# Kernel optimization log

Measured on AMD Instinct MI355X. Metric: run time of the kernel, lower is better.

## Reference

```python
import jax, jax.numpy as jnp
import numpy as np

N = 10000      # num_nodes
E = 80000      # num_edges
IN = 256       # input_dim
T = 768        # text_embedding_dim
H1, H2 = 1024, 1024
HEADS = 4
ND = 100       # num_domains
NS = 10000     # num_skills
SD = 128       # skill_dim
B = 1024       # skill batch
K = 20         # skills per set
LN_EPS = 1e-5
COS_EPS = 1e-8
NEG_SLOPE = 0.2


def setup_inputs() -> dict:
    key = jax.random.key(0)
    ks = jax.random.split(key, 64)
    r = lambda i, shape, s=0.02: jax.random.normal(ks[i], shape, jnp.float32) * s
    inp = {}
    inp['x'] = jax.random.normal(ks[0], (N, IN), jnp.float32)
    inp['edge_index'] = jax.random.randint(ks[1], (2, E), 0, N)
    inp['domain_ids'] = jax.random.randint(ks[2], (N,), 0, ND)
    inp['skill_ids_1'] = jax.random.randint(ks[3], (B, K), 0, NS)
    inp['skill_ids_2'] = jax.random.randint(ks[4], (B, K), 0, NS)
    for j, name in enumerate(['bio', 'expertise', 'needs', 'goals']):
        inp[name + '_embeddings'] = jax.random.normal(ks[5 + j], (N, T), jnp.float32)
        inp[name + '_w'] = r(9 + 2 * j, (T, T))
        inp[name + '_b'] = jnp.zeros((T,), jnp.float32)
    dims = [IN + 4 * T, H1, H2]
    for i in range(2):
        din, dout = dims[i], dims[i + 1]
        base = 20 + 8 * i
        inp[f'gcn_w{i}'] = r(base, (din, dout))
        inp[f'gcn_b{i}'] = jnp.zeros((dout,), jnp.float32)
        inp[f'gat_w{i}'] = r(base + 1, (dout, dout))
        inp[f'gat_as{i}'] = r(base + 2, (HEADS, dout // HEADS), 0.1)
        inp[f'gat_ad{i}'] = r(base + 3, (HEADS, dout // HEADS), 0.1)
        inp[f'gat_b{i}'] = jnp.zeros((dout,), jnp.float32)
        inp[f'ln_g{i}'] = jnp.ones((dout,), jnp.float32)
        inp[f'ln_b{i}'] = jnp.zeros((dout,), jnp.float32)
    inp['dom_emb'] = r(40, (ND, H2), 1.0)
    inp['dom_w'] = r(41, (H2, H2))
    inp['dom_b'] = jnp.zeros((H2,), jnp.float32)
    inp['skill_emb'] = r(42, (NS, SD), 1.0)
    inp['c_w1'] = r(43, (2 * SD, H2))
    inp['c_b1'] = jnp.zeros((H2,), jnp.float32)
    inp['c_w2'] = r(44, (H2, 1))
    inp['c_b2'] = jnp.zeros((1,), jnp.float32)
    return inp


def _layernorm(x, g, b):
    m = x.mean(-1, keepdims=True)
    v = ((x - m) ** 2).mean(-1, keepdims=True)
    return (x - m) * jax.lax.rsqrt(v + LN_EPS) * g + b


def _gcn(x, src, dst, W, b, n):
    # PyG GCNConv: self loops already in (src,dst); symmetric normalization
    xw = x @ W
    deg = jnp.zeros((n,), x.dtype).at[dst].add(1.0)
    dinv = jax.lax.rsqrt(jnp.maximum(deg, 1.0))  # deg >= 1 due to self loops
    norm = dinv[src] * dinv[dst]                 # [Etot]
    out = jnp.zeros_like(xw).at[dst].add(norm[:, None] * xw[src])
    return out + b


def _gat(x, src, dst, W, a_s, a_d, b, n, heads):
    c = W.shape[1] // heads
    h = (x @ W).reshape(n, heads, c)             # [N,H,C]
    es = jnp.einsum('nhc,hc->nh', h, a_s)
    ed = jnp.einsum('nhc,hc->nh', h, a_d)
    e = jax.nn.leaky_relu(es[src] + ed[dst], NEG_SLOPE)   # [Etot,H]
    m = jnp.full((n, heads), -jnp.inf, x.dtype).at[dst].max(e)
    ee = jnp.exp(e - m[dst])
    s = jnp.zeros((n, heads), x.dtype).at[dst].add(ee)
    alpha = ee / s[dst]                          # segment softmax over dst
    out = jnp.zeros((n, heads, c), x.dtype).at[dst].add(alpha[..., None] * h[src])
    return out.reshape(n, heads * c) + b


def _cos(a, b):
    na = jnp.maximum(jnp.linalg.norm(a, axis=-1), COS_EPS)
    nb = jnp.maximum(jnp.linalg.norm(b, axis=-1), COS_EPS)
    return (a * b).sum(-1) / (na * nb)


def _forward(x, edge_index, domain_ids, skill_ids_1, skill_ids_2,
             bio_embeddings, bio_w, bio_b,
             expertise_embeddings, expertise_w, expertise_b,
             needs_embeddings, needs_w, needs_b,
             goals_embeddings, goals_w, goals_b,
             gcn_w0, gcn_b0, gat_w0, gat_as0, gat_ad0, gat_b0, ln_g0, ln_b0,
             gcn_w1, gcn_b1, gat_w1, gat_as1, gat_ad1, gat_b1, ln_g1, ln_b1,
             dom_emb, dom_w, dom_b, skill_emb, c_w1, c_b1, c_w2, c_b2):
    n = x.shape[0]
    bio_f = bio_embeddings @ bio_w + bio_b
    exp_f = expertise_embeddings @ expertise_w + expertise_b
    needs_f = needs_embeddings @ needs_w + needs_b
    goals_f = goals_embeddings @ goals_w + goals_b
    combined = jnp.concatenate([x, bio_f, exp_f, needs_f, goals_f], axis=1)

    src, dst = edge_index[0], edge_index[1]
    loops = jnp.arange(n)
    srcl = jnp.concatenate([src, loops])   # self loops (GCN & GAT both add them)
    dstl = jnp.concatenate([dst, loops])

    h = combined
    layers = [(gcn_w0, gcn_b0, gat_w0, gat_as0, gat_ad0, gat_b0, ln_g0, ln_b0),
              (gcn_w1, gcn_b1, gat_w1, gat_as1, gat_ad1, gat_b1, ln_g1, ln_b1)]
    for (gw, gb, aw, a_s, a_d, ab, lg, lb) in layers:
        x_gcn = _gcn(h, srcl, dstl, gw, gb, n)
        x_att = _gat(x_gcn, srcl, dstl, aw, a_s, a_d, ab, n, HEADS)
        h = jax.nn.relu(_layernorm(x_att + x_gcn, lg, lb))

    domain_embeddings = h @ dom_w + dom_b + dom_emb[domain_ids]

    s1 = skill_emb[skill_ids_1].mean(axis=1)   # [B,SD]
    s2 = skill_emb[skill_ids_2].mean(axis=1)
    comb = jnp.concatenate([s1, s2], axis=1)
    compat = jax.nn.sigmoid(jax.nn.relu(comb @ c_w1 + c_b1) @ c_w2 + c_b2)

    bio_sim = _cos(bio_f[src], bio_f[dst])
    en_sim = _cos(exp_f[src], needs_f[dst])
    ne_sim = _cos(needs_f[src], exp_f[dst])
    goals_sim = _cos(goals_f[src], goals_f[dst])
    return domain_embeddings, compat, bio_sim, en_sim, ne_sim, goals_sim


def reference(x, edge_index, domain_ids, skill_ids_1, skill_ids_2,
              bio_embeddings, bio_w, bio_b,
              expertise_embeddings, expertise_w, expertise_b,
              needs_embeddings, needs_w, needs_b,
              goals_embeddings, goals_w, goals_b,
              gcn_w0, gcn_b0, gat_w0, gat_as0, gat_ad0, gat_b0, ln_g0, ln_b0,
              gcn_w1, gcn_b1, gat_w1, gat_as1, gat_ad1, gat_b1, ln_g1, ln_b1,
              dom_emb, dom_w, dom_b, skill_emb, c_w1, c_b1, c_w2, c_b2):
    return _forward(x, edge_index, domain_ids, skill_ids_1, skill_ids_2,
                    bio_embeddings, bio_w, bio_b,
                    expertise_embeddings, expertise_w, expertise_b,
                    needs_embeddings, needs_w, needs_b,
                    goals_embeddings, goals_w, goals_b,
                    gcn_w0, gcn_b0, gat_w0, gat_as0, gat_ad0, gat_b0, ln_g0, ln_b0,
                    gcn_w1, gcn_b1, gat_w1, gat_as1, gat_ad1, gat_b1, ln_g1, ln_b1,
                    dom_emb, dom_w, dom_b, skill_emb, c_w1, c_b1, c_w2, c_b2)
```

## Files before the change

kernel.cpp:

```cpp
#include <hip/hip_runtime.h>
#include <math.h>

typedef unsigned short u16;
typedef unsigned short u16x4 __attribute__((ext_vector_type(4)));
typedef unsigned short u16x8 __attribute__((ext_vector_type(8)));
typedef short s16x8 __attribute__((ext_vector_type(8)));
typedef float f32x4 __attribute__((ext_vector_type(4)));

constexpr int NN   = 10000;
constexpr int MP   = 10112;
constexpr int IN   = 256;
constexpr int TD   = 768;
constexpr int CD   = 3328;
constexpr int HD   = 1024;
constexpr int HCH  = 256;
constexpr int SDIM = 128;
constexpr int KSK  = 20;
constexpr int ACAP = 256;
constexpr float LN_EPS = 1e-5f;
constexpr float COS_EPS = 1e-8f;
constexpr float NEG_SLOPE = 0.2f;

__device__ __forceinline__ float warp_sum(float v){
#pragma unroll
  for (int o=1;o<64;o<<=1) v += __shfl_xor(v,o);
  return v;
}
__device__ __forceinline__ float warp_max(float v){
#pragma unroll
  for (int o=1;o<64;o<<=1) v = fmaxf(v, __shfl_xor(v,o));
  return v;
}
__device__ __forceinline__ u16 f2b(float f){
  unsigned u = __float_as_uint(f);
  return (u16)((u + 0x7fffu + ((u>>16)&1u)) >> 16);
}
__device__ __forceinline__ float b2f(u16 b){ return __uint_as_float(((unsigned)b)<<16); }

#define GLDS(g, l) __builtin_amdgcn_global_load_lds( \
    (const __attribute__((address_space(1))) void*)(g), \
    (__attribute__((address_space(3))) void*)(l), 16, 0, 0)

__global__ __launch_bounds__(256) void k_gemm_bf16(
    const u16* __restrict__ A, long Az,
    const u16* __restrict__ B0c, const u16* __restrict__ B1c,
    const u16* __restrict__ B2c, const u16* __restrict__ B3c,
    const float* __restrict__ bias0, const float* __restrict__ bias1,
    const float* __restrict__ bias2, const float* __restrict__ bias3,
    float* __restrict__ Cf, int ldcf,
    u16* __restrict__ Cb, int ldcb, long Cbz,
    const float* __restrict__ demb, const int* __restrict__ dids,
    int M, int K, int relu)
{
  __shared__ __align__(16) u16 smem[16384];
  const int z = blockIdx.z;
  const u16* Bt = (z==0)? B0c : (z==1)? B1c : (z==2)? B2c : B3c;
  const float* bias = (z==0)? bias0 : (z==1)? bias1 : (z==2)? bias2 : bias3;
  const u16* Ab = A + (size_t)z * (size_t)Az;

  const int tid = threadIdx.x;
  const int wave = tid >> 6, lane = tid & 63;
  const int wr = wave >> 1, wc = wave & 1;

  const int nwg  = gridDim.x * gridDim.y;
  const int orig = blockIdx.y * gridDim.x + blockIdx.x;
  const int q = nwg >> 3, r = nwg & 7;
  const int xcd = orig & 7, loc = orig >> 3;
  const int wg = (xcd < r ? xcd*(q+1) : r*(q+1) + (xcd-r)*q) + loc;
  const int bx = wg % gridDim.x, byy = wg / gridDim.x;
  const size_t bm = (size_t)byy * 128;
  const size_t bn = (size_t)bx * 128;

  f32x4 acc[4][4];
#pragma unroll
  for (int m=0;m<4;m++)
#pragma unroll
    for (int n=0;n<4;n++) acc[m][n] = f32x4{0.f,0.f,0.f,0.f};

  const int srow = tid >> 2;
  const int scol = (tid & 3) * 8;
  const u16* ga0 = Ab + (bm + srow) * (size_t)K + scol;
  const u16* ga1 = ga0 + (size_t)64 * K;
  const u16* gb0 = Bt + (bn + srow) * (size_t)K + scol;
  const u16* gb1 = gb0 + (size_t)64 * K;

  auto stage = [&](int buf, int k0){
    GLDS(ga0 + k0, smem + buf*4096 + wave*512);
    GLDS(ga1 + k0, smem + buf*4096 + 2048 + wave*512);
    GLDS(gb0 + k0, smem + 8192 + buf*4096 + wave*512);
    GLDS(gb1 + k0, smem + 8192 + buf*4096 + 2048 + wave*512);
  };

  const int ar = wr*64 + (lane & 15);
  const int br = wc*64 + (lane & 15);
  const int kg = (lane >> 4) * 8;

  const int nt = K >> 5;
  stage(0, 0);
  __syncthreads();
  int cur = 0;
  for (int t = 0; t < nt; ++t){
    if (t+1 < nt) stage(cur^1, (t+1)*32);
    s16x8 a[4], b[4];
#pragma unroll
    for (int m=0;m<4;m++) a[m] = *(const s16x8*)(smem + cur*4096 + (ar + m*16)*32 + kg);
#pragma unroll
    for (int n=0;n<4;n++) b[n] = *(const s16x8*)(smem + 8192 + cur*4096 + (br + n*16)*32 + kg);
#pragma unroll
    for (int m=0;m<4;m++)
#pragma unroll
      for (int n=0;n<4;n++)
        acc[m][n] = __builtin_amdgcn_mfma_f32_16x16x32_bf16(a[m], b[n], acc[m][n], 0, 0, 0);
    __syncthreads();
    cur ^= 1;
  }

  const int cl0 = wc*64 + (lane & 15);
  if (Cb){
#pragma unroll
    for (int m=0;m<4;m++)
#pragma unroll
      for (int j=0;j<4;j++){
        int rl = wr*64 + ((lane >> 4) * 4) + m*16 + j;
#pragma unroll
        for (int n=0;n<4;n++){
          int cl = cl0 + n*16;
          float v = acc[m][n][j];
          if (bias) v += bias[bn + cl];
          if (relu) v = fmaxf(v, 0.f);
          smem[rl*128 + cl] = f2b(v);
        }
      }
    __syncthreads();
#pragma unroll
    for (int it=0; it<8; ++it){
      int rl = it*16 + (tid >> 4);
      int cl = (tid & 15) * 8;
      u16x8 vv = *(const u16x8*)(smem + rl*128 + cl);
      *(u16x8*)(Cb + (size_t)z*Cbz + (bm + rl)*(size_t)ldcb + bn + cl) = vv;
    }
  } else if (Cf){
    float* ctf = (float*)smem;
#pragma unroll
    for (int p=0;p<2;p++){
      if (wr == p){
#pragma unroll
        for (int m=0;m<4;m++)
#pragma unroll
          for (int j=0;j<4;j++){
            int rl = ((lane >> 4) * 4) + m*16 + j;
            int rg = (int)bm + p*64 + rl;
            const float* dbase = (demb && rg < M) ? demb + (size_t)dids[rg]*HD : nullptr;
#pragma unroll
            for (int n=0;n<4;n++){
              int cl = cl0 + n*16;
              float v = acc[m][n][j];
              if (bias) v += bias[bn + cl];
              if (dbase) v += dbase[bn + cl];
              if (relu) v = fmaxf(v, 0.f);
              ctf[rl*128 + cl] = v;
            }
          }
      }
      __syncthreads();
#pragma unroll
      for (int it=0; it<8; ++it){
        int rl = it*8 + (tid >> 5);
        int cl = (tid & 31) * 4;
        int rg = (int)bm + p*64 + rl;
        if (rg < M){
          float4 vv = *(const float4*)(ctf + rl*128 + cl);
          *(float4*)(Cf + (size_t)rg*ldcf + bn + cl) = vv;
        }
      }
      __syncthreads();
    }
  }
}

__global__ void k_f2b8x4(const float* __restrict__ s0, const float* __restrict__ s1,
                         const float* __restrict__ s2, const float* __restrict__ s3,
                         u16* __restrict__ out, long per, long ostride){
  int z = blockIdx.y;
  const float* s = (z==0)? s0 : (z==1)? s1 : (z==2)? s2 : s3;
  long i = ((long)blockIdx.x*256 + threadIdx.x)*8;
  if (i >= per) return;
  float4 v0 = *(const float4*)(s+i);
  float4 v1 = *(const float4*)(s+i+4);
  u16x8 o;
  o[0]=f2b(v0.x); o[1]=f2b(v0.y); o[2]=f2b(v0.z); o[3]=f2b(v0.w);
  o[4]=f2b(v1.x); o[5]=f2b(v1.y); o[6]=f2b(v1.z); o[7]=f2b(v1.w);
  *(u16x8*)(out + z*ostride + i) = o;
}

__global__ void k_copyx_b(const float* __restrict__ x, u16* __restrict__ comb){
  long i = ((long)blockIdx.x*256 + threadIdx.x)*8;
  int n = (int)(i >> 8), c = (int)(i & 255);
  float4 v0 = *(const float4*)(x+i);
  float4 v1 = *(const float4*)(x+i+4);
  u16x8 o;
  o[0]=f2b(v0.x); o[1]=f2b(v0.y); o[2]=f2b(v0.z); o[3]=f2b(v0.w);
  o[4]=f2b(v1.x); o[5]=f2b(v1.y); o[6]=f2b(v1.z); o[7]=f2b(v1.w);
  *(u16x8*)(comb + (size_t)n*CD + c) = o;
}

__global__ __launch_bounds__(256) void k_transb4(
    const float* __restrict__ B0c, const float* __restrict__ B1c,
    const float* __restrict__ B2c, const float* __restrict__ B3c,
    u16* __restrict__ T0, u16* __restrict__ T1,
    u16* __restrict__ T2, u16* __restrict__ T3, int K, int N){
  __shared__ u16 tile[32][40];
  int z = blockIdx.z;
  const float* B = (z==0)? B0c : (z==1)? B1c : (z==2)? B2c : B3c;
  u16* Bt = (z==0)? T0 : (z==1)? T1 : (z==2)? T2 : T3;
  int n0 = blockIdx.x*32, k0 = blockIdx.y*32;
  int tx = threadIdx.x & 31, ty = threadIdx.x >> 5;
#pragma unroll
  for (int i=0;i<4;i++)
    tile[ty+8*i][tx] = f2b(B[(size_t)(k0+ty+8*i)*N + n0+tx]);
  __syncthreads();
#pragma unroll
  for (int i=0;i<4;i++)
    Bt[(size_t)(n0+ty+8*i)*K + k0+tx] = tile[tx][ty+8*i];
}

__global__ void k_hist(const int* __restrict__ dst, int* __restrict__ indeg, int E){
  int e = blockIdx.x*256 + threadIdx.x;
  if (e < E) atomicAdd(&indeg[dst[e]], 1);
}

__global__ __launch_bounds__(1024) void k_scan(const int* __restrict__ indeg,
    int* __restrict__ row_start, int* __restrict__ cursor,
    float* __restrict__ dinv, int Nn)
{
  __shared__ int wsum[16];
  __shared__ int carry_s;
  int t = threadIdx.x, wave = t >> 6, lane = t & 63;
  if (t==0) carry_s = 0;
  __syncthreads();
  for (int base=0; base<Nn; base+=1024) {
    int i = base + t;
    int v = (i<Nn)? indeg[i] : 0;
    int s = v;
#pragma unroll
    for (int o=1;o<64;o<<=1){ int tmp = __shfl_up(s, o); if (lane>=o) s += tmp; }
    if (lane==63) wsum[wave] = s;
    __syncthreads();
    if (wave==0 && lane<16){
      int w = wsum[lane];
#pragma unroll
      for (int o=1;o<16;o<<=1){ int tmp = __shfl_up(w, o); if (lane>=o) w += tmp; }
      wsum[lane] = w;
    }
    __syncthreads();
    int woff = (wave==0)? 0 : wsum[wave-1];
    int incl = s + woff;
    int carry = carry_s;
    if (i<Nn){
      int ex = carry + incl - v;
      row_start[i]=ex; cursor[i]=ex;
      dinv[i] = rsqrtf((float)(v + 1));
    }
    __syncthreads();
    if (t==1023) carry_s = carry + incl;
    __syncthreads();
  }
  if (t==0) row_start[Nn] = carry_s;
}

__global__ void k_scatter(const int* __restrict__ src, const int* __restrict__ dst,
    int* __restrict__ cursor, int* __restrict__ csr_src,
    int* __restrict__ csr_eid, int E){
  int e = blockIdx.x*256 + threadIdx.x;
  if (e < E){
    int d = dst[e];
    int pos = atomicAdd(&cursor[d], 1);
    csr_src[pos] = src[e];
    csr_eid[pos] = e;
  }
}

__global__ __launch_bounds__(128) void k_gcn_agg(
    const u16* __restrict__ xw, const int* __restrict__ row_start,
    const int* __restrict__ csr_src, const float* __restrict__ dinv,
    const float* __restrict__ bias, u16* __restrict__ outb)
{
  int d = blockIdx.x, t = threadIdx.x;
  int c0 = t*8;
  float di = dinv[d];
  u16x8 sv = *(const u16x8*)(xw + (size_t)d*HD + c0);
  float acc[8];
#pragma unroll
  for (int i=0;i<8;i++) acc[i] = di*di*b2f(sv[i]);
  int beg = row_start[d], end = row_start[d+1];
  int j = beg;
  for (; j+4 <= end; j += 4){
    int s0=csr_src[j], s1=csr_src[j+1], s2=csr_src[j+2], s3=csr_src[j+3];
    u16x8 r0 = *(const u16x8*)(xw + (size_t)s0*HD + c0);
    u16x8 r1 = *(const u16x8*)(xw + (size_t)s1*HD + c0);
    u16x8 r2 = *(const u16x8*)(xw + (size_t)s2*HD + c0);
    u16x8 r3 = *(const u16x8*)(xw + (size_t)s3*HD + c0);
    float w0=di*dinv[s0], w1=di*dinv[s1], w2=di*dinv[s2], w3=di*dinv[s3];
#pragma unroll
    for (int i=0;i<8;i++){
      acc[i] = fmaf(w0, b2f(r0[i]), acc[i]);
      acc[i] = fmaf(w1, b2f(r1[i]), acc[i]);
      acc[i] = fmaf(w2, b2f(r2[i]), acc[i]);
      acc[i] = fmaf(w3, b2f(r3[i]), acc[i]);
    }
  }
  for (; j<end; ++j){
    int s = csr_src[j];
    float w = di*dinv[s];
    u16x8 rv = *(const u16x8*)(xw + (size_t)s*HD + c0);
#pragma unroll
    for (int i=0;i<8;i++) acc[i] = fmaf(w, b2f(rv[i]), acc[i]);
  }
  float4 bv0 = *(const float4*)(bias + c0);
  float4 bv1 = *(const float4*)(bias + c0 + 4);
  float o[8] = {acc[0]+bv0.x, acc[1]+bv0.y, acc[2]+bv0.z, acc[3]+bv0.w,
                acc[4]+bv1.x, acc[5]+bv1.y, acc[6]+bv1.z, acc[7]+bv1.w};
  u16x8 ob;
#pragma unroll
  for (int i=0;i<8;i++) ob[i]=f2b(o[i]);
  *(u16x8*)(outb + (size_t)d*HD + c0) = ob;
}

__global__ __launch_bounds__(256) void k_es_ed(
    const u16* __restrict__ hw, const float* __restrict__ a_s,
    const float* __restrict__ a_d, float* __restrict__ es, float* __restrict__ ed)
{
  int n = blockIdx.x; int wv = threadIdx.x >> 6; int lane = threadIdx.x & 63;
  u16x4 v  = *(const u16x4*)(hw + (size_t)n*HD + wv*HCH + lane*4);
  float4 as = *(const float4*)(a_s + wv*HCH + lane*4);
  float4 ad = *(const float4*)(a_d + wv*HCH + lane*4);
  float f0=b2f(v[0]), f1=b2f(v[1]), f2v=b2f(v[2]), f3=b2f(v[3]);
  float ss = f0*as.x + f1*as.y + f2v*as.z + f3*as.w;
  float sd = f0*ad.x + f1*ad.y + f2v*ad.z + f3*ad.w;
  ss = warp_sum(ss); sd = warp_sum(sd);
  if (lane==0){ es[n*4+wv]=ss; ed[n*4+wv]=sd; }
}

__global__ __launch_bounds__(128) void k_gat_fused(
    const u16* __restrict__ hw, const int* __restrict__ row_start,
    const int* __restrict__ csr_src, const float* __restrict__ es,
    const float* __restrict__ ed, const float* __restrict__ bias,
    const u16* __restrict__ gcn, const float* __restrict__ g,
    const float* __restrict__ b, u16* __restrict__ out)
{
  __shared__ float4 alph[ACAP];
  __shared__ float xch[8];
  int d = blockIdx.x, t = threadIdx.x, wv = t>>6, lane = t&63;
  int beg = row_start[d], end = row_start[d+1], deg = end-beg;
  float4 edq = *(const float4*)(ed + (size_t)d*4);
  float4 esq = *(const float4*)(es + (size_t)d*4);
  float edv[4] = {edq.x,edq.y,edq.z,edq.w};
  float esv[4] = {esq.x,esq.y,esq.z,esq.w};
  float eself[4], m[4];
#pragma unroll
  for (int h=0;h<4;h++){
    float e = esv[h] + edv[h];
    eself[h] = (e>0.f)? e : NEG_SLOPE*e;
    m[h] = eself[h];
  }
  for (int j=beg+t; j<end; j+=128){
    int s = csr_src[j];
    float4 qv = *(const float4*)(es + (size_t)s*4);
    float qa[4] = {qv.x,qv.y,qv.z,qv.w};
#pragma unroll
    for (int h=0;h<4;h++){
      float e = qa[h]+edv[h]; e = (e>0.f)? e : NEG_SLOPE*e;
      m[h] = fmaxf(m[h], e);
    }
  }
#pragma unroll
  for (int h=0;h<4;h++) m[h] = warp_max(m[h]);
  if (lane==0) ((float4*)xch)[wv] = make_float4(m[0],m[1],m[2],m[3]);
  __syncthreads();
  {
    float4 m0 = ((float4*)xch)[0], m1 = ((float4*)xch)[1];
    m[0]=fmaxf(m0.x,m1.x); m[1]=fmaxf(m0.y,m1.y);
    m[2]=fmaxf(m0.z,m1.z); m[3]=fmaxf(m0.w,m1.w);
  }
  __syncthreads();
  bool fits = (deg <= ACAP);
  float sum[4] = {0.f,0.f,0.f,0.f};
  for (int j=beg+t; j<end; j+=128){
    int s = csr_src[j];
    float4 qv = *(const float4*)(es + (size_t)s*4);
    float qa[4] = {qv.x,qv.y,qv.z,qv.w}, p[4];
#pragma unroll
    for (int h=0;h<4;h++){
      float e = qa[h]+edv[h]; e = (e>0.f)? e : NEG_SLOPE*e;
      p[h] = expf(e-m[h]); sum[h]+=p[h];
    }
    if (fits) alph[j-beg] = make_float4(p[0],p[1],p[2],p[3]);
  }
#pragma unroll
  for (int h=0;h<4;h++) sum[h]=warp_sum(sum[h]);
  if (lane==0) ((float4*)xch)[wv] = make_float4(sum[0],sum[1],sum[2],sum[3]);
  __syncthreads();
  float rsm[4], swt[4];
  {
    float4 s0=((float4*)xch)[0], s1=((float4*)xch)[1];
    float sa[4] = {s0.x+s1.x, s0.y+s1.y, s0.z+s1.z, s0.w+s1.w};
#pragma unroll
    for (int h=0;h<4;h++){
      float pe = expf(eself[h]-m[h]);
      rsm[h] = 1.f/(sa[h]+pe);
      swt[h] = pe*rsm[h];
    }
  }
  int c0 = t*8, h0 = t>>5;
  u16x8 sv = *(const u16x8*)(hw + (size_t)d*HD + c0);
  float acc[8];
#pragma unroll
  for (int i=0;i<8;i++) acc[i] = swt[h0]*b2f(sv[i]);
  float mh = m[h0], rh = rsm[h0], edh = edv[h0];
  if (fits){
    int j = beg;
    for (; j+4 <= end; j += 4){
      int s0=csr_src[j], s1=csr_src[j+1], s2=csr_src[j+2], s3=csr_src[j+3];
      u16x8 r0 = *(const u16x8*)(hw + (size_t)s0*HD + c0);
      u16x8 r1 = *(const u16x8*)(hw + (size_t)s1*HD + c0);
      u16x8 r2 = *(const u16x8*)(hw + (size_t)s2*HD + c0);
      u16x8 r3 = *(const u16x8*)(hw + (size_t)s3*HD + c0);
      float a0 = ((const float*)&alph[j-beg  ])[h0] * rh;
      float a1 = ((const float*)&alph[j-beg+1])[h0] * rh;
      float a2 = ((const float*)&alph[j-beg+2])[h0] * rh;
      float a3 = ((const float*)&alph[j-beg+3])[h0] * rh;
#pragma unroll
      for (int i=0;i<8;i++){
        acc[i] = fmaf(a0, b2f(r0[i]), acc[i]);
        acc[i] = fmaf(a1, b2f(r1[i]), acc[i]);
        acc[i] = fmaf(a2, b2f(r2[i]), acc[i]);
        acc[i] = fmaf(a3, b2f(r3[i]), acc[i]);
      }
    }
    for (; j<end; ++j){
      int s = csr_src[j];
      float av = ((const float*)&alph[j-beg])[h0] * rh;
      u16x8 rv = *(const u16x8*)(hw + (size_t)s*HD + c0);
#pragma unroll
      for (int i=0;i<8;i++) acc[i] = fmaf(av, b2f(rv[i]), acc[i]);
    }
  } else {
    for (int j=beg; j<end; ++j){
      int s = csr_src[j];
      float e = es[(size_t)s*4+h0] + edh; e = (e>0.f)? e : NEG_SLOPE*e;
      float av = expf(e-mh)*rh;
      u16x8 rv = *(const u16x8*)(hw + (size_t)s*HD + c0);
#pragma unroll
      for (int i=0;i<8;i++) acc[i] = fmaf(av, b2f(rv[i]), acc[i]);
    }
  }
  float4 bv0 = *(const float4*)(bias + c0), bv1 = *(const float4*)(bias + c0 + 4);
  u16x8 gv = *(const u16x8*)(gcn + (size_t)d*HD + c0);
  float ba8[8] = {bv0.x,bv0.y,bv0.z,bv0.w,bv1.x,bv1.y,bv1.z,bv1.w};
  float xv[8];
#pragma unroll
  for (int i=0;i<8;i++) xv[i] = acc[i] + ba8[i] + b2f(gv[i]);
  float ssum=0.f, ssq=0.f;
#pragma unroll
  for (int i=0;i<8;i++){ ssum += xv[i]; ssq = fmaf(xv[i], xv[i], ssq); }
  ssum = warp_sum(ssum); ssq = warp_sum(ssq);
  __syncthreads();
  if (lane==0){ xch[wv]=ssum; xch[2+wv]=ssq; }
  __syncthreads();
  ssum = xch[0]+xch[1]; ssq = xch[2]+xch[3];
  float mean = ssum * (1.f/HD);
  float var  = ssq * (1.f/HD) - mean*mean;
  float rsln = rsqrtf(var + LN_EPS);
  float4 gg0 = *(const float4*)(g + c0), gg1 = *(const float4*)(g + c0 + 4);
  float4 bb0 = *(const float4*)(b + c0), bb1 = *(const float4*)(b + c0 + 4);
  float ga[8] = {gg0.x,gg0.y,gg0.z,gg0.w,gg1.x,gg1.y,gg1.z,gg1.w};
  float ba[8] = {bb0.x,bb0.y,bb0.z,bb0.w,bb1.x,bb1.y,bb1.z,bb1.w};
  u16x8 ob;
#pragma unroll
  for (int i=0;i<8;i++)
    ob[i] = f2b(fmaxf((xv[i]-mean)*rsln*ga[i] + ba[i], 0.f));
  *(u16x8*)(out + (size_t)d*HD + c0) = ob;
}

__global__ __launch_bounds__(256) void k_sims_csr(
    const u16* __restrict__ comb,
    const int* __restrict__ row_start, const int* __restrict__ csr_src,
    const int* __restrict__ csr_eid, float* __restrict__ out, int E)
{
  int d = blockIdx.x;
  int w = threadIdx.x>>6, lane = threadIdx.x&63;
  int g = lane>>4, l = lane&15;
  int beg = row_start[d], end = row_start[d+1];
  if (beg >= end) return;
  const int baseA[4] = {IN, IN+TD,   IN+2*TD, IN+3*TD};
  const int baseB[4] = {IN, IN+2*TD, IN+TD,   IN+3*TD};
  const u16* bp = comb + (size_t)d*CD + baseB[g] + l*8;
  float bf[48];
  float nbss = 0.f;
#pragma unroll
  for (int i=0;i<6;i++){
    u16x8 v = *(const u16x8*)(bp + i*128);
#pragma unroll
    for (int k=0;k<8;k++){
      float f = b2f(v[k]);
      bf[i*8+k] = f;
      nbss = fmaf(f, f, nbss);
    }
  }
  nbss += __shfl_xor(nbss,1); nbss += __shfl_xor(nbss,2);
  nbss += __shfl_xor(nbss,4); nbss += __shfl_xor(nbss,8);
  float rnb = 1.f / fmaxf(sqrtf(nbss), COS_EPS);
  for (int j = beg + w; j < end; j += 4){
    int s = csr_src[j];
    const u16* ap = comb + (size_t)s*CD + baseA[g] + l*8;
    float dot = 0.f, ass = 0.f;
#pragma unroll
    for (int i=0;i<6;i++){
      u16x8 v = *(const u16x8*)(ap + i*128);
#pragma unroll
      for (int k=0;k<8;k++){
        float f = b2f(v[k]);
        dot = fmaf(f, bf[i*8+k], dot);
        ass = fmaf(f, f, ass);
      }
    }
    dot += __shfl_xor(dot,1); dot += __shfl_xor(dot,2);
    dot += __shfl_xor(dot,4); dot += __shfl_xor(dot,8);
    ass += __shfl_xor(ass,1); ass += __shfl_xor(ass,2);
    ass += __shfl_xor(ass,4); ass += __shfl_xor(ass,8);
    if (l==0){
      float na = fmaxf(sqrtf(ass), COS_EPS);
      out[(size_t)g*E + csr_eid[j]] = dot * rnb / na;
    }
  }
}

__global__ __launch_bounds__(128) void k_skill_mean_b(
    const float* __restrict__ semb, const int* __restrict__ id1,
    const int* __restrict__ id2, u16* __restrict__ comb)
{
  int b = blockIdx.x, c = threadIdx.x;
  float s1=0.f, s2=0.f;
  for (int k=0;k<KSK;k++){
    s1 += semb[(size_t)id1[b*KSK+k]*SDIM + c];
    s2 += semb[(size_t)id2[b*KSK+k]*SDIM + c];
  }
  comb[(size_t)b*256 + c]       = f2b(s1*(1.f/KSK));
  comb[(size_t)b*256 + 128 + c] = f2b(s2*(1.f/KSK));
}

__global__ __launch_bounds__(256) void k_compat(
    const float* __restrict__ hidden, const float* __restrict__ w2,
    const float* __restrict__ b2, float* __restrict__ out)
{
  __shared__ float red[4];
  int bi = blockIdx.x, t = threadIdx.x;
  float s = 0.f;
  for (int c=t;c<HD;c+=256) s = fmaf(hidden[(size_t)bi*HD+c], w2[c], s);
  s = warp_sum(s);
  if ((t&63)==0) red[t>>6] = s;
  __syncthreads();
  if (t==0){
    float tot = red[0]+red[1]+red[2]+red[3] + b2[0];
    out[bi] = 1.f/(1.f+expf(-tot));
  }
}

extern "C" void kernel_launch(void* const* d_in, const int* in_sizes, int n_in,
                              void* d_out, int out_size, void* d_ws, size_t ws_size,
                              hipStream_t stream)
{
  const float* x         = (const float*)d_in[0];
  const int*   eidx      = (const int*)d_in[1];
  const int*   dom_ids   = (const int*)d_in[2];
  const int*   sk1       = (const int*)d_in[3];
  const int*   sk2       = (const int*)d_in[4];
  const float* bio_emb   = (const float*)d_in[5];
  const float* bio_w     = (const float*)d_in[6];
  const float* bio_b     = (const float*)d_in[7];
  const float* exp_emb   = (const float*)d_in[8];
  const float* exp_w     = (const float*)d_in[9];
  const float* exp_b     = (const float*)d_in[10];
  const float* needs_emb = (const float*)d_in[11];
  const float* needs_w   = (const float*)d_in[12];
  const float* needs_b   = (const float*)d_in[13];
  const float* goals_emb = (const float*)d_in[14];
  const float* goals_w   = (const float*)d_in[15];
  const float* goals_b   = (const float*)d_in[16];
  const float* gcn_w0 = (const float*)d_in[17];
  const float* gcn_b0 = (const float*)d_in[18];
  const float* gat_w0 = (const float*)d_in[19];
  const float* gat_as0= (const float*)d_in[20];
  const float* gat_ad0= (const float*)d_in[21];
  const float* gat_b0 = (const float*)d_in[22];
  const float* ln_g0  = (const float*)d_in[23];
  const float* ln_b0  = (const float*)d_in[24];
  const float* gcn_w1 = (const float*)d_in[25];
  const float* gcn_b1 = (const float*)d_in[26];
  const float* gat_w1 = (const float*)d_in[27];
  const float* gat_as1= (const float*)d_in[28];
  const float* gat_ad1= (const float*)d_in[29];
  const float* gat_b1 = (const float*)d_in[30];
  const float* ln_g1  = (const float*)d_in[31];
  const float* ln_b1  = (const float*)d_in[32];
  const float* dom_emb= (const float*)d_in[33];
  const float* dom_w  = (const float*)d_in[34];
  const float* dom_b  = (const float*)d_in[35];
  const float* skill_emb = (const float*)d_in[36];
  const float* c_w1   = (const float*)d_in[37];
  const float* c_b1   = (const float*)d_in[38];
  const float* c_w2   = (const float*)d_in[39];
  const float* c_b2   = (const float*)d_in[40];

  const int E   = in_sizes[1] / 2;
  const int Bsz = in_sizes[3] / KSK;
  const int* srcp = eidx;
  const int* dstp = eidx + E;

  char* wsp = (char*)d_ws;
  size_t off = 0;
  auto alloc = [&](size_t bytes)->void*{
    void* p = wsp + off;
    off += (bytes + 255) & ~(size_t)255;
    return p;
  };
  u16*   combined_b = (u16*)alloc((size_t)MP*CD*2);
  u16*   Aact       = (u16*)alloc((size_t)4*MP*TD*2);
  u16*   P0b  = (u16*) alloc((size_t)MP*HD*2);
  u16*   P1b  = (u16*) alloc((size_t)MP*HD*2);
  u16*   Rh   = (u16*) alloc((size_t)MP*HD*2);
  u16*   wt_bio   = (u16*)alloc((size_t)TD*TD*2);
  u16*   wt_exp   = (u16*)alloc((size_t)TD*TD*2);
  u16*   wt_needs = (u16*)alloc((size_t)TD*TD*2);
  u16*   wt_goals = (u16*)alloc((size_t)TD*TD*2);
  u16*   w_gcn0t  = (u16*)alloc((size_t)HD*CD*2);
  u16*   w_gat0t  = (u16*)alloc((size_t)HD*HD*2);
  u16*   w_gcn1t  = (u16*)alloc((size_t)HD*HD*2);
  u16*   w_gat1t  = (u16*)alloc((size_t)HD*HD*2);
  u16*   w_domt   = (u16*)alloc((size_t)HD*HD*2);
  u16*   w_c1t    = (u16*)alloc((size_t)HD*2*SDIM*2);
  u16*   comb_b   = (u16*)alloc((size_t)Bsz*2*SDIM*2);
  float* hidden   = (float*)alloc((size_t)Bsz*HD*4);
  float* es      = (float*)alloc((size_t)NN*4*4);
  float* ed      = (float*)alloc((size_t)NN*4*4);
  float* dinv    = (float*)alloc((size_t)NN*4);
  int*   indeg   = (int*)  alloc((size_t)NN*4);
  int*   row_st  = (int*)  alloc((size_t)(NN+1)*4);
  int*   cursor  = (int*)  alloc((size_t)NN*4);
  int*   csr_src = (int*)  alloc((size_t)E*4);
  int*   csr_eid = (int*)  alloc((size_t)E*4);

  u16* Rhwb = combined_b;

  float* out0       = (float*)d_out;
  float* out_compat = out0 + (size_t)NN*HD;
  float* out_sims   = out_compat + Bsz;

  dim3 blk(256);

  hipMemsetAsync(indeg, 0, (size_t)NN*sizeof(int), stream);
  k_hist<<<dim3((E+255)/256), blk, 0, stream>>>(dstp, indeg, E);
  k_scan<<<dim3(1), dim3(1024), 0, stream>>>(indeg, row_st, cursor, dinv, NN);
  k_scatter<<<dim3((E+255)/256), blk, 0, stream>>>(srcp, dstp, cursor, csr_src, csr_eid, E);

  k_transb4<<<dim3(TD/32, TD/32, 4), blk, 0, stream>>>(
      bio_w, exp_w, needs_w, goals_w, wt_bio, wt_exp, wt_needs, wt_goals, TD, TD);
  k_transb4<<<dim3(HD/32, HD/32, 4), blk, 0, stream>>>(
      gat_w0, gcn_w1, gat_w1, dom_w, w_gat0t, w_gcn1t, w_gat1t, w_domt, HD, HD);
  k_transb4<<<dim3(HD/32, CD/32, 1), blk, 0, stream>>>(
      gcn_w0, gcn_w0, gcn_w0, gcn_w0, w_gcn0t, w_gcn0t, w_gcn0t, w_gcn0t, CD, HD);
  k_transb4<<<dim3(HD/32, (2*SDIM)/32, 1), blk, 0, stream>>>(
      c_w1, c_w1, c_w1, c_w1, w_c1t, w_c1t, w_c1t, w_c1t, 2*SDIM, HD);

  k_copyx_b<<<dim3((NN*IN)/8/256), blk, 0, stream>>>(x, combined_b);
  k_f2b8x4<<<dim3((NN*TD)/8/256, 4), blk, 0, stream>>>(
      bio_emb, exp_emb, needs_emb, goals_emb, Aact, (long)NN*TD, (long)MP*TD);
  k_gemm_bf16<<<dim3(TD/128, MP/128, 4), blk, 0, stream>>>(
      Aact, (long)MP*TD, wt_bio, wt_exp, wt_needs, wt_goals,
      bio_b, exp_b, needs_b, goals_b,
      nullptr, 0, combined_b + IN, CD, (long)TD,
      nullptr, nullptr, NN, TD, 0);

  k_sims_csr<<<dim3(NN), blk, 0, stream>>>(combined_b, row_st, csr_src,
                                           csr_eid, out_sims, E);

  k_skill_mean_b<<<dim3(Bsz), dim3(128), 0, stream>>>(skill_emb, sk1, sk2, comb_b);
  k_gemm_bf16<<<dim3(HD/128, Bsz/128, 1), blk, 0, stream>>>(
      comb_b, 0, w_c1t, w_c1t, w_c1t, w_c1t, c_b1, c_b1, c_b1, c_b1,
      hidden, HD, nullptr, 0, 0, nullptr, nullptr, Bsz, 2*SDIM, 1);
  k_compat<<<dim3(Bsz), blk, 0, stream>>>(hidden, c_w2, c_b2, out_compat);

  dim3 g_h(HD/128, MP/128, 1);

  k_gemm_bf16<<<g_h, blk, 0, stream>>>(
      combined_b, 0, w_gcn0t, w_gcn0t, w_gcn0t, w_gcn0t,
      nullptr, nullptr, nullptr, nullptr,
      nullptr, 0, P0b, HD, 0, nullptr, nullptr, NN, CD, 0);
  k_gcn_agg<<<dim3(NN), dim3(128), 0, stream>>>(P0b, row_st, csr_src, dinv, gcn_b0, P1b);
  k_gemm_bf16<<<g_h, blk, 0, stream>>>(
      P1b, 0, w_gat0t, w_gat0t, w_gat0t, w_gat0t,
      nullptr, nullptr, nullptr, nullptr,
      nullptr, 0, Rhwb, HD, 0, nullptr, nullptr, NN, HD, 0);
  k_es_ed<<<dim3(NN), blk, 0, stream>>>(Rhwb, gat_as0, gat_ad0, es, ed);
  k_gat_fused<<<dim3(NN), dim3(128), 0, stream>>>(Rhwb, row_st, csr_src, es, ed,
                                                  gat_b0, P1b, ln_g0, ln_b0, Rh);

  k_gemm_bf16<<<g_h, blk, 0, stream>>>(
      Rh, 0, w_gcn1t, w_gcn1t, w_gcn1t, w_gcn1t,
      nullptr, nullptr, nullptr, nullptr,
      nullptr, 0, P0b, HD, 0, nullptr, nullptr, NN, HD, 0);
  k_gcn_agg<<<dim3(NN), dim3(128), 0, stream>>>(P0b, row_st, csr_src, dinv, gcn_b1, P1b);
  k_gemm_bf16<<<g_h, blk, 0, stream>>>(
      P1b, 0, w_gat1t, w_gat1t, w_gat1t, w_gat1t,
      nullptr, nullptr, nullptr, nullptr,
      nullptr, 0, Rhwb, HD, 0, nullptr, nullptr, NN, HD, 0);
  k_es_ed<<<dim3(NN), blk, 0, stream>>>(Rhwb, gat_as1, gat_ad1, es, ed);
  k_gat_fused<<<dim3(NN), dim3(128), 0, stream>>>(Rhwb, row_st, csr_src, es, ed,
                                                  gat_b1, P1b, ln_g1, ln_b1, Rh);

  k_gemm_bf16<<<g_h, blk, 0, stream>>>(
      Rh, 0, w_domt, w_domt, w_domt, w_domt,
      dom_b, dom_b, dom_b, dom_b,
      out0, HD, nullptr, 0, 0, dom_emb, dom_ids, NN, HD, 0);
}
```

Baseline: 642.3 us.

## Fuse fp32-to-bf16 conversion of text embeddings into the text projection GEMM

Removes the separate kernel that converted the four fp32 text embedding matrices to bf16 into a staging buffer. A new GEMM loads fp32 A tiles directly into registers, converts them to bf16 and writes them to shared memory while B is staged asynchronously, double-buffered. This saves a full write and reread of the bf16 activation copy and one launch. In exchange, the A loads now go through registers instead of direct-to-LDS loads, which may reduce the GEMM's own efficiency. The A-tile fetch also reads twice as many bytes per element from global memory.

```diff
diff --git a/kernel.cpp b/kernel.cpp
--- a/kernel.cpp
+++ b/kernel.cpp
@@ -178,19 +178,116 @@
   }
 }
 
-__global__ void k_f2b8x4(const float* __restrict__ s0, const float* __restrict__ s1,
-                         const float* __restrict__ s2, const float* __restrict__ s3,
-                         u16* __restrict__ out, long per, long ostride){
-  int z = blockIdx.y;
-  const float* s = (z==0)? s0 : (z==1)? s1 : (z==2)? s2 : s3;
-  long i = ((long)blockIdx.x*256 + threadIdx.x)*8;
-  if (i >= per) return;
-  float4 v0 = *(const float4*)(s+i);
-  float4 v1 = *(const float4*)(s+i+4);
-  u16x8 o;
-  o[0]=f2b(v0.x); o[1]=f2b(v0.y); o[2]=f2b(v0.z); o[3]=f2b(v0.w);
-  o[4]=f2b(v1.x); o[5]=f2b(v1.y); o[6]=f2b(v1.z); o[7]=f2b(v1.w);
-  *(u16x8*)(out + z*ostride + i) = o;
+__global__ __launch_bounds__(256) void k_gemm_text(
+    const float* __restrict__ A0, const float* __restrict__ A1,
+    const float* __restrict__ A2, const float* __restrict__ A3,
+    const u16* __restrict__ B0c, const u16* __restrict__ B1c,
+    const u16* __restrict__ B2c, const u16* __restrict__ B3c,
+    const float* __restrict__ bias0, const float* __restrict__ bias1,
+    const float* __restrict__ bias2, const float* __restrict__ bias3,
+    u16* __restrict__ Cb, int ldcb, long Cbz, int M, int K)
+{
+  __shared__ __align__(16) u16 smem[16384];
+  const int z = blockIdx.z;
+  const float* Af = (z==0)? A0 : (z==1)? A1 : (z==2)? A2 : A3;
+  const u16* Bt = (z==0)? B0c : (z==1)? B1c : (z==2)? B2c : B3c;
+  const float* bias = (z==0)? bias0 : (z==1)? bias1 : (z==2)? bias2 : bias3;
+
+  const int tid = threadIdx.x;
+  const int wave = tid >> 6, lane = tid & 63;
+  const int wr = wave >> 1, wc = wave & 1;
+
+  const int nwg  = gridDim.x * gridDim.y;
+  const int orig = blockIdx.y * gridDim.x + blockIdx.x;
+  const int q = nwg >> 3, r = nwg & 7;
+  const int xcd = orig & 7, loc = orig >> 3;
+  const int wg = (xcd < r ? xcd*(q+1) : r*(q+1) + (xcd-r)*q) + loc;
+  const int bx = wg % gridDim.x, byy = wg / gridDim.x;
+  const size_t bm = (size_t)byy * 128;
+  const size_t bn = (size_t)bx * 128;
+
+  f32x4 acc[4][4];
+#pragma unroll
+  for (int m=0;m<4;m++)
+#pragma unroll
+    for (int n=0;n<4;n++) acc[m][n] = f32x4{0.f,0.f,0.f,0.f};
+
+  const int srow = tid >> 2;
+  const int scol = (tid & 3) * 8;
+  const u16* gb0 = Bt + (bn + srow) * (size_t)K + scol;
+  const u16* gb1 = gb0 + (size_t)64 * K;
+  auto stageB = [&](int buf, int k0){
+    GLDS(gb0 + k0, smem + 8192 + buf*4096 + wave*512);
+    GLDS(gb1 + k0, smem + 8192 + buf*4096 + 2048 + wave*512);
+  };
+
+  const int r0l = tid >> 1;
+  const int c0l = (tid & 1) * 16;
+  int rr = (int)bm + r0l; if (rr > M-1) rr = M-1;
+  const float* ga = Af + (size_t)rr * (size_t)K + c0l;
+
+  float4 av0, av1, av2, av3;
+  auto ldA = [&](int k0){
+    av0 = *(const float4*)(ga + k0);
+    av1 = *(const float4*)(ga + k0 + 4);
+    av2 = *(const float4*)(ga + k0 + 8);
+    av3 = *(const float4*)(ga + k0 + 12);
+  };
+  auto wrA = [&](int buf){
+    u16x8 o0, o1;
+    o0[0]=f2b(av0.x); o0[1]=f2b(av0.y); o0[2]=f2b(av0.z); o0[3]=f2b(av0.w);
+    o0[4]=f2b(av1.x); o0[5]=f2b(av1.y); o0[6]=f2b(av1.z); o0[7]=f2b(av1.w);
+    o1[0]=f2b(av2.x); o1[1]=f2b(av2.y); o1[2]=f2b(av2.z); o1[3]=f2b(av2.w);
+    o1[4]=f2b(av3.x); o1[5]=f2b(av3.y); o1[6]=f2b(av3.z); o1[7]=f2b(av3.w);
+    *(u16x8*)(smem + buf*4096 + r0l*32 + c0l)     = o0;
+    *(u16x8*)(smem + buf*4096 + r0l*32 + c0l + 8) = o1;
+  };
+
+  const int ar = wr*64 + (lane & 15);
+  const int br = wc*64 + (lane & 15);
+  const int kg = (lane >> 4) * 8;
+
+  const int nt = K >> 5;
+  ldA(0); stageB(0, 0); wrA(0);
+  __syncthreads();
+  int cur = 0;
+  for (int t = 0; t < nt; ++t){
+    if (t+1 < nt){ ldA((t+1)*32); stageB(cur^1, (t+1)*32); }
+    s16x8 a[4], b[4];
+#pragma unroll
+    for (int m=0;m<4;m++) a[m] = *(const s16x8*)(smem + cur*4096 + (ar + m*16)*32 + kg);
+#pragma unroll
+    for (int n=0;n<4;n++) b[n] = *(const s16x8*)(smem + 8192 + cur*4096 + (br + n*16)*32 + kg);
+#pragma unroll
+    for (int m=0;m<4;m++)
+#pragma unroll
+      for (int n=0;n<4;n++)
+        acc[m][n] = __builtin_amdgcn_mfma_f32_16x16x32_bf16(a[m], b[n], acc[m][n], 0, 0, 0);
+    if (t+1 < nt) wrA(cur^1);
+    __syncthreads();
+    cur ^= 1;
+  }
+
+  const int cl0 = wc*64 + (lane & 15);
+#pragma unroll
+  for (int m=0;m<4;m++)
+#pragma unroll
+    for (int j=0;j<4;j++){
+      int rl = wr*64 + ((lane >> 4) * 4) + m*16 + j;
+#pragma unroll
+      for (int n=0;n<4;n++){
+        int cl = cl0 + n*16;
+        smem[rl*128 + cl] = f2b(acc[m][n][j] + bias[bn + cl]);
+      }
+    }
+  __syncthreads();
+#pragma unroll
+  for (int it=0; it<8; ++it){
+    int rl = it*16 + (tid >> 4);
+    int cl = (tid & 15) * 8;
+    u16x8 vv = *(const u16x8*)(smem + rl*128 + cl);
+    *(u16x8*)(Cb + (size_t)z*Cbz + (bm + rl)*(size_t)ldcb + bn + cl) = vv;
+  }
 }
 
 __global__ void k_copyx_b(const float* __restrict__ x, u16* __restrict__ comb){
@@ -625,7 +722,6 @@
     return p;
   };
   u16*   combined_b = (u16*)alloc((size_t)MP*CD*2);
-  u16*   Aact       = (u16*)alloc((size_t)4*MP*TD*2);
   u16*   P0b  = (u16*) alloc((size_t)MP*HD*2);
   u16*   P1b  = (u16*) alloc((size_t)MP*HD*2);
   u16*   Rh   = (u16*) alloc((size_t)MP*HD*2);
@@ -673,13 +769,11 @@
       c_w1, c_w1, c_w1, c_w1, w_c1t, w_c1t, w_c1t, w_c1t, 2*SDIM, HD);
 
   k_copyx_b<<<dim3((NN*IN)/8/256), blk, 0, stream>>>(x, combined_b);
-  k_f2b8x4<<<dim3((NN*TD)/8/256, 4), blk, 0, stream>>>(
-      bio_emb, exp_emb, needs_emb, goals_emb, Aact, (long)NN*TD, (long)MP*TD);
-  k_gemm_bf16<<<dim3(TD/128, MP/128, 4), blk, 0, stream>>>(
-      Aact, (long)MP*TD, wt_bio, wt_exp, wt_needs, wt_goals,
+  k_gemm_text<<<dim3(TD/128, MP/128, 4), blk, 0, stream>>>(
+      bio_emb, exp_emb, needs_emb, goals_emb,
+      wt_bio, wt_exp, wt_needs, wt_goals,
       bio_b, exp_b, needs_b, goals_b,
-      nullptr, 0, combined_b + IN, CD, (long)TD,
-      nullptr, nullptr, NN, TD, 0);
+      combined_b + IN, CD, (long)TD, NN, TD);
 
   k_sims_csr<<<dim3(NN), blk, 0, stream>>>(combined_b, row_st, csr_src,
                                            csr_eid, out_sims, E);
```

Measured after the change: 632.6 us. Within noise of the previous version (-1.5%).
